# Optimization experiments

Measured on AMD Instinct MI355X. Metric: run time of the kernel, lower is better.

The kernel has to match this reference:

```python
import jax, jax.numpy as jnp
import numpy as np

N_NODES = 50000
N_EDGES = 1600000
N_GRAPHS = 512
HID = 32
NEG_SLOPE = 0.2  # PyG GATConv default leaky_relu slope
EPS = 1e-16      # PyG softmax denominator epsilon


def setup_inputs() -> dict:
    key = jax.random.key(0)
    ks = jax.random.split(key, 12)
    x = jax.random.normal(ks[0], (N_NODES, 12), jnp.float32)
    edge_index = jax.random.randint(ks[1], (2, N_EDGES), 0, N_NODES)
    edge_attr = jax.random.normal(ks[2], (N_EDGES, 3), jnp.float32)
    batch = jnp.sort(jax.random.randint(ks[3], (N_NODES,), 0, N_GRAPHS))
    g = lambda k, shp: jax.random.normal(k, shp, jnp.float32) * (1.0 / np.sqrt(shp[0]))
    return {
        "x": x, "edge_index": edge_index, "edge_attr": edge_attr, "batch": batch,
        "W": g(ks[4], (12, HID)),
        "att_src": g(ks[5], (HID,)), "att_dst": g(ks[6], (HID,)),
        "W_edge": g(ks[7], (3, HID)), "att_edge": g(ks[8], (HID,)),
        "bias": jnp.zeros((HID,), jnp.float32),
        "W_gate": g(ks[9], (HID, 1)), "b_gate": jnp.zeros((1,), jnp.float32),
        "W_out": g(ks[10], (HID, 1)), "b_out": jnp.zeros((1,), jnp.float32),
    }


def reference(x, edge_index, edge_attr, batch, W, att_src, att_dst, W_edge,
              att_edge, bias, W_gate, b_gate, W_out, b_out):
    N = x.shape[0]
    src, dst = edge_index[0], edge_index[1]

    # --- add self loops, edge_attr fill_value='mean' (mean of incoming edge attrs per node)
    deg = jax.ops.segment_sum(jnp.ones_like(edge_attr[:, 0]), dst, num_segments=N)
    loop_attr = jax.ops.segment_sum(edge_attr, dst, num_segments=N) / jnp.maximum(deg, 1.0)[:, None]
    loop = jnp.arange(N, dtype=src.dtype)
    src_f = jnp.concatenate([src, loop])
    dst_f = jnp.concatenate([dst, loop])
    ea = jnp.concatenate([edge_attr, loop_attr], axis=0)  # [E+N, 3]

    # --- GATConv (heads=1)
    h = x @ W                       # [N, HID]
    a_src = h @ att_src             # [N]
    a_dst = h @ att_dst             # [N]
    a_edge = (ea @ W_edge) @ att_edge  # [E+N]
    alpha = jax.nn.leaky_relu(a_src[src_f] + a_dst[dst_f] + a_edge, NEG_SLOPE)
    # segment softmax over destination neighborhoods
    m = jax.ops.segment_max(alpha, dst_f, num_segments=N)
    e = jnp.exp(alpha - m[dst_f])
    z = jax.ops.segment_sum(e, dst_f, num_segments=N)
    alpha = e / (z[dst_f] + EPS)
    out = jax.ops.segment_sum(h[src_f] * alpha[:, None], dst_f, num_segments=N) + bias

    out = jax.nn.relu(out)  # dropout is identity in eval mode

    # --- GlobalAttention pooling: gate = softmax(Linear(out), batch)
    gate = (out @ W_gate + b_gate)[:, 0]  # [N]
    gm = jax.ops.segment_max(gate, batch, num_segments=N_GRAPHS)
    ge = jnp.exp(gate - gm[batch])
    gz = jax.ops.segment_sum(ge, batch, num_segments=N_GRAPHS)
    gate = ge / (gz[batch] + EPS)
    pooled = jax.ops.segment_sum(out * gate[:, None], batch, num_segments=N_GRAPHS)  # [G, HID]

    return jax.nn.sigmoid(pooled @ W_out + b_out)  # [G, 1]
```

## Files before the change

kernel.cpp:

```cpp
#include <hip/hip_runtime.h>
#include <hip/hip_fp16.h>
#include <math.h>

#define N_NODES 50000
#define N_EDGES 1600000
#define N_GRAPHS 512
#define HID 32
#define NEG_SLOPE 0.2f
#define SM_EPS 1e-16f
#define PAD 80
#define NBIN 511
#define BIN_W 98
#define BIN_CAP 3800
#define EPT 10
#define PART_BLOCKS 313
#define MAXG 8

__global__ __launch_bounds__(512) void k_part_node(const int* __restrict__ ei,
                                                   const float* __restrict__ ea,
                                                   const float* __restrict__ W_edge,
                                                   const float* __restrict__ att_edge,
                                                   const float* __restrict__ x,
                                                   const float* __restrict__ W,
                                                   const float* __restrict__ att_src,
                                                   const float* __restrict__ att_dst,
                                                   uint2* __restrict__ part,
                                                   int* __restrict__ pcur,
                                                   __half2* __restrict__ h2,
                                                   float* __restrict__ a_src,
                                                   float* __restrict__ a_dst) {
    __shared__ float sv[3];
    __shared__ float sW[12 * 32], sas[32], sad[32];
    __shared__ int lcnt[NBIN], lcur[NBIN];
    int t = threadIdx.x;
    if (t < 3) {
        float v = 0.f;
        for (int j = 0; j < 32; ++j) v += W_edge[t * 32 + j] * att_edge[j];
        sv[t] = v;
    }
    for (int i = t; i < 12 * 32; i += 512) sW[i] = W[i];
    if (t < 32) { sas[t] = att_src[t]; sad[t] = att_dst[t]; }
    for (int i = t; i < NBIN; i += 512) lcnt[i] = 0;
    __syncthreads();

    uint2 r[EPT];
    int bin[EPT];
    int ebase = blockIdx.x * (512 * EPT) + t;
#pragma unroll
    for (int i = 0; i < EPT; ++i) {
        int e = ebase + i * 512;
        if (e < N_EDGES) {
            int s = ei[e];
            int d = ei[N_EDGES + e];
            float aev = ea[e * 3 + 0] * sv[0] + ea[e * 3 + 1] * sv[1] + ea[e * 3 + 2] * sv[2];
            r[i] = make_uint2((unsigned)d | ((unsigned)s << 16), __float_as_uint(aev));
            bin[i] = d / BIN_W;
            atomicAdd(&lcnt[bin[i]], 1);
        } else {
            bin[i] = -1;
        }
    }
    __syncthreads();
    for (int i = t; i < NBIN; i += 512) lcur[i] = atomicAdd(pcur + i, lcnt[i]);
    __syncthreads();
#pragma unroll
    for (int i = 0; i < EPT; ++i) {
        if (bin[i] >= 0) {
            int pos = atomicAdd(&lcur[bin[i]], 1);
            if (pos < BIN_CAP) part[(size_t)bin[i] * BIN_CAP + pos] = r[i];
        }
    }

    int n = blockIdx.x * 160 + t;
    if (t < 160 && n < N_NODES) {
        float xv[12];
#pragma unroll
        for (int j = 0; j < 12; ++j) xv[j] = x[n * 12 + j];
        float hv[32];
        float as = 0.f, ad = 0.f;
#pragma unroll
        for (int k = 0; k < 32; ++k) {
            float acc = 0.f;
#pragma unroll
            for (int j = 0; j < 12; ++j) acc += xv[j] * sW[j * 32 + k];
            hv[k] = acc;
            as += acc * sas[k];
            ad += acc * sad[k];
        }
        a_src[n] = as;
        a_dst[n] = ad;
        __half2 hp[16];
#pragma unroll
        for (int k = 0; k < 16; ++k) hp[k] = __floats2half2_rn(hv[2 * k], hv[2 * k + 1]);
        uint4* dst = (uint4*)(h2 + (size_t)n * 16);
        const uint4* srcp = (const uint4*)hp;
#pragma unroll
        for (int k = 0; k < 4; ++k) dst[k] = srcp[k];
    }
}

__global__ __launch_bounds__(1024) void k_asm_gather(const uint2* __restrict__ part,
                                                     const int* __restrict__ pcur,
                                                     const __half2* __restrict__ h2,
                                                     const float* __restrict__ a_src,
                                                     const float* __restrict__ a_dst,
                                                     const float* __restrict__ bias,
                                                     const float* __restrict__ W_gate,
                                                     const float* __restrict__ b_gate,
                                                     const int* __restrict__ batch,
                                                     float* __restrict__ Sg,
                                                     float* __restrict__ gzg) {
    int b = blockIdx.x;
    int lo = b * BIN_W;
    if (lo >= N_NODES) return;
    int hi = lo + BIN_W; if (hi > N_NODES) hi = N_NODES;
    int nrow = hi - lo;
    __shared__ int lcur[BIN_W];
    __shared__ unsigned lbuck[BIN_W * PAD];
    __shared__ float S_local[MAXG][32];
    __shared__ float gz_local[MAXG];
    __shared__ int sgf, sgl;
    int t = threadIdx.x;
    if (t < BIN_W) lcur[t] = 0;
    if (t < MAXG * 32) S_local[t >> 5][t & 31] = 0.f;
    if (t < MAXG) gz_local[t] = 0.f;
    if (t == 0) { sgf = batch[lo]; sgl = batch[hi - 1]; }
    __syncthreads();
    int gfirst = sgf;

    int cnt = pcur[b]; if (cnt > BIN_CAP) cnt = BIN_CAP;
    const uint2* p = part + (size_t)b * BIN_CAP;
    for (int i = t; i < cnt; i += 1024) {
        uint2 r = p[i];
        int li = (int)(r.x & 0xFFFF) - lo;
        unsigned s = r.x >> 16;
        unsigned short hb = __half_as_ushort(__float2half_rn(__uint_as_float(r.y)));
        int pos = atomicAdd(&lcur[li], 1);
        if (pos < PAD) lbuck[li * PAD + pos] = s | ((unsigned)hb << 16);
    }
    __syncthreads();

    int l = t & 63, wl = t >> 6;
    int es = l >> 2;
    int cg = l & 3;
    float bg0 = b_gate[0];

    for (int li = wl; li < nrow; li += 16) {
        int n = lo + li;
        int deg_full = lcur[li];
        int degc = deg_full < PAD ? deg_full : PAD;
        float adst_n = a_dst[n];
        const unsigned* row = lbuck + li * PAD;

        float c0 = 0.f, c1 = 0.f, c2 = 0.f, c3 = 0.f, c4 = 0.f, c5 = 0.f, c6 = 0.f, c7 = 0.f;
        float wsum = 0.f, aevsum = 0.f;
        int j = es;
        for (; j + 16 < degc; j += 32) {
            unsigned p0 = row[j], p1 = row[j + 16];
            int s0 = p0 & 0xFFFF, s1 = p1 & 0xFFFF;
            float aev0 = __half2float(__ushort_as_half((unsigned short)(p0 >> 16)));
            float aev1 = __half2float(__ushort_as_half((unsigned short)(p1 >> 16)));
            float as0 = a_src[s0], as1 = a_src[s1];
            const uint4 u0 = *(const uint4*)(h2 + (size_t)s0 * 16 + cg * 4);
            const uint4 u1 = *(const uint4*)(h2 + (size_t)s1 * 16 + cg * 4);
            float a0 = as0 + adst_n + aev0; a0 = a0 > 0.f ? a0 : NEG_SLOPE * a0;
            float a1 = as1 + adst_n + aev1; a1 = a1 > 0.f ? a1 : NEG_SLOPE * a1;
            float w0 = __expf(a0), w1 = __expf(a1);
            wsum += w0 + w1; aevsum += aev0 + aev1;
            float2 f;
            f = __half22float2(*(const __half2*)&u0.x); c0 += w0 * f.x; c1 += w0 * f.y;
            f = __half22float2(*(const __half2*)&u0.y); c2 += w0 * f.x; c3 += w0 * f.y;
            f = __half22float2(*(const __half2*)&u0.z); c4 += w0 * f.x; c5 += w0 * f.y;
            f = __half22float2(*(const __half2*)&u0.w); c6 += w0 * f.x; c7 += w0 * f.y;
            f = __half22float2(*(const __half2*)&u1.x); c0 += w1 * f.x; c1 += w1 * f.y;
            f = __half22float2(*(const __half2*)&u1.y); c2 += w1 * f.x; c3 += w1 * f.y;
            f = __half22float2(*(const __half2*)&u1.z); c4 += w1 * f.x; c5 += w1 * f.y;
            f = __half22float2(*(const __half2*)&u1.w); c6 += w1 * f.x; c7 += w1 * f.y;
        }
        if (j < degc) {
            unsigned p0 = row[j];
            int s0 = p0 & 0xFFFF;
            float aev0 = __half2float(__ushort_as_half((unsigned short)(p0 >> 16)));
            float a0 = a_src[s0] + adst_n + aev0; a0 = a0 > 0.f ? a0 : NEG_SLOPE * a0;
            float w0 = __expf(a0);
            const uint4 u0 = *(const uint4*)(h2 + (size_t)s0 * 16 + cg * 4);
            wsum += w0; aevsum += aev0;
            float2 f;
            f = __half22float2(*(const __half2*)&u0.x); c0 += w0 * f.x; c1 += w0 * f.y;
            f = __half22float2(*(const __half2*)&u0.y); c2 += w0 * f.x; c3 += w0 * f.y;
            f = __half22float2(*(const __half2*)&u0.z); c4 += w0 * f.x; c5 += w0 * f.y;
            f = __half22float2(*(const __half2*)&u0.w); c6 += w0 * f.x; c7 += w0 * f.y;
        }

#pragma unroll
        for (int m = 4; m <= 32; m <<= 1) {
            c0 += __shfl_xor(c0, m); c1 += __shfl_xor(c1, m);
            c2 += __shfl_xor(c2, m); c3 += __shfl_xor(c3, m);
            c4 += __shfl_xor(c4, m); c5 += __shfl_xor(c5, m);
            c6 += __shfl_xor(c6, m); c7 += __shfl_xor(c7, m);
            wsum += __shfl_xor(wsum, m); aevsum += __shfl_xor(aevsum, m);
        }

        float dgm = deg_full > 1 ? (float)deg_full : 1.f;
        float al = a_src[n] + adst_n + aevsum / dgm;
        al = al > 0.f ? al : NEG_SLOPE * al;
        float el = __expf(al);
        float zi = 1.f / (wsum + el + SM_EPS);

        if (es == 0) {
            const uint4 un = *(const uint4*)(h2 + (size_t)n * 16 + cg * 4);
            float hn[8];
            float2 f;
            f = __half22float2(*(const __half2*)&un.x); hn[0] = f.x; hn[1] = f.y;
            f = __half22float2(*(const __half2*)&un.y); hn[2] = f.x; hn[3] = f.y;
            f = __half22float2(*(const __half2*)&un.z); hn[4] = f.x; hn[5] = f.y;
            f = __half22float2(*(const __half2*)&un.w); hn[6] = f.x; hn[7] = f.y;
            const float4 bva = *(const float4*)(bias + cg * 8);
            const float4 bvb = *(const float4*)(bias + cg * 8 + 4);
            float v[8];
            v[0] = (c0 + el * hn[0]) * zi + bva.x;
            v[1] = (c1 + el * hn[1]) * zi + bva.y;
            v[2] = (c2 + el * hn[2]) * zi + bva.z;
            v[3] = (c3 + el * hn[3]) * zi + bva.w;
            v[4] = (c4 + el * hn[4]) * zi + bvb.x;
            v[5] = (c5 + el * hn[5]) * zi + bvb.y;
            v[6] = (c6 + el * hn[6]) * zi + bvb.z;
            v[7] = (c7 + el * hn[7]) * zi + bvb.w;
#pragma unroll
            for (int k = 0; k < 8; ++k) v[k] = v[k] > 0.f ? v[k] : 0.f;
            const float4 wga = *(const float4*)(W_gate + cg * 8);
            const float4 wgb = *(const float4*)(W_gate + cg * 8 + 4);
            float g = v[0] * wga.x + v[1] * wga.y + v[2] * wga.z + v[3] * wga.w
                    + v[4] * wgb.x + v[5] * wgb.y + v[6] * wgb.z + v[7] * wgb.w;
            g += __shfl_xor(g, 1);
            g += __shfl_xor(g, 2);
            float gen = __expf(g + bg0);
            int gi = batch[n] - gfirst; gi = gi < MAXG - 1 ? gi : MAXG - 1;
#pragma unroll
            for (int k = 0; k < 8; ++k) atomicAdd(&S_local[gi][cg * 8 + k], gen * v[k]);
            if (cg == 0) atomicAdd(&gz_local[gi], gen);
        }
    }
    __syncthreads();

    int ngr = sgl - gfirst + 1; if (ngr > MAXG) ngr = MAXG;
    for (int i = t; i < ngr * 33; i += 1024) {
        int q = i / 33, c = i % 33;
        if (c < 32) atomicAdd(&Sg[(size_t)(gfirst + q) * 32 + c], S_local[q][c]);
        else atomicAdd(&gzg[gfirst + q], gz_local[q]);
    }
}

__global__ __launch_bounds__(256) void k_out(const float* __restrict__ Sg,
                                             const float* __restrict__ gzg,
                                             const float* __restrict__ W_out,
                                             const float* __restrict__ b_out,
                                             float* __restrict__ out) {
    int g = blockIdx.x * blockDim.x + threadIdx.x;
    if (g >= N_GRAPHS) return;
    float zi = 1.f / (gzg[g] + SM_EPS);
    float acc = b_out[0];
#pragma unroll
    for (int k = 0; k < 32; ++k) acc += Sg[(size_t)g * 32 + k] * zi * W_out[k];
    out[g] = 1.f / (1.f + __expf(-acc));
}

extern "C" void kernel_launch(void* const* d_in, const int* in_sizes, int n_in,
                              void* d_out, int out_size, void* d_ws, size_t ws_size,
                              hipStream_t stream) {
    const float* x        = (const float*)d_in[0];
    const int*   ei       = (const int*)  d_in[1];
    const float* ea       = (const float*)d_in[2];
    const int*   batch    = (const int*)  d_in[3];
    const float* W        = (const float*)d_in[4];
    const float* att_src  = (const float*)d_in[5];
    const float* att_dst  = (const float*)d_in[6];
    const float* W_edge   = (const float*)d_in[7];
    const float* att_edge = (const float*)d_in[8];
    const float* bias     = (const float*)d_in[9];
    const float* W_gate   = (const float*)d_in[10];
    const float* b_gate   = (const float*)d_in[11];
    const float* W_out    = (const float*)d_in[12];
    const float* b_out    = (const float*)d_in[13];
    float* out = (float*)d_out;

    char* wsb = (char*)d_ws;
    uint2*    part_  = (uint2*)wsb;
    __half2*  h2     = (__half2*)(part_ + (size_t)NBIN * BIN_CAP);
    float*    a_src  = (float*)(h2 + (size_t)16 * N_NODES);
    float*    a_dst  = a_src + N_NODES;
    float*    Sg     = a_dst + N_NODES;
    float*    gzg    = Sg + (size_t)N_GRAPHS * 32;
    int*      pcur   = (int*)(gzg + N_GRAPHS);

    size_t zero_bytes = ((size_t)N_GRAPHS * 33 + NBIN) * sizeof(float);
    hipMemsetAsync(Sg, 0, zero_bytes, stream);

    k_part_node<<<PART_BLOCKS, 512, 0, stream>>>(ei, ea, W_edge, att_edge, x, W, att_src,
                                                 att_dst, part_, pcur, h2, a_src, a_dst);
    k_asm_gather<<<NBIN, 1024, 0, stream>>>(part_, pcur, h2, a_src, a_dst, bias,
                                            W_gate, b_gate, batch, Sg, gzg);
    k_out<<<(N_GRAPHS + 255) / 256, 256, 0, stream>>>(Sg, gzg, W_out, b_out, out);
}
```

Measured before the change: 167.7 us.

## Stage partitioned edges in shared memory via local scan before global scatter

Each block now records a per-edge rank within its bin, prefix-scans the bin counts, and writes its edges into a shared-memory buffer sorted by bin. It then copies them to the global partition array with consecutive threads writing consecutive slots of a bin. The aim is to replace scattered 8-byte global writes with more coalesced runs and to drop the second round of shared atomics. The cost is about 40KB of extra shared memory, which may lower occupancy, plus a log-step scan with many barriers.

```diff
diff --git a/kernel.cpp b/kernel.cpp
--- a/kernel.cpp
+++ b/kernel.cpp
@@ -13,6 +13,7 @@
 #define BIN_W 98
 #define BIN_CAP 3800
 #define EPT 10
+#define EPB 5120
 #define PART_BLOCKS 313
 #define MAXG 8
 
@@ -31,7 +32,9 @@
                                                    float* __restrict__ a_dst) {
     __shared__ float sv[3];
     __shared__ float sW[12 * 32], sas[32], sad[32];
-    __shared__ int lcnt[NBIN], lcur[NBIN];
+    __shared__ int lcnt[NBIN], lbase[NBIN], lcur[NBIN];
+    __shared__ int sscan[512];
+    __shared__ uint2 sbuf[EPB];
     int t = threadIdx.x;
     if (t < 3) {
         float v = 0.f;
@@ -40,12 +43,12 @@
     }
     for (int i = t; i < 12 * 32; i += 512) sW[i] = W[i];
     if (t < 32) { sas[t] = att_src[t]; sad[t] = att_dst[t]; }
-    for (int i = t; i < NBIN; i += 512) lcnt[i] = 0;
+    if (t < NBIN) lcnt[t] = 0;
     __syncthreads();
 
     uint2 r[EPT];
-    int bin[EPT];
-    int ebase = blockIdx.x * (512 * EPT) + t;
+    int bin[EPT], rank[EPT];
+    int ebase = blockIdx.x * EPB + t;
 #pragma unroll
     for (int i = 0; i < EPT; ++i) {
         int e = ebase + i * 512;
@@ -55,20 +58,39 @@
             float aev = ea[e * 3 + 0] * sv[0] + ea[e * 3 + 1] * sv[1] + ea[e * 3 + 2] * sv[2];
             r[i] = make_uint2((unsigned)d | ((unsigned)s << 16), __float_as_uint(aev));
             bin[i] = d / BIN_W;
-            atomicAdd(&lcnt[bin[i]], 1);
+            rank[i] = atomicAdd(&lcnt[bin[i]], 1);
         } else {
             bin[i] = -1;
         }
     }
     __syncthreads();
-    for (int i = t; i < NBIN; i += 512) lcur[i] = atomicAdd(pcur + i, lcnt[i]);
-    __syncthreads();
-#pragma unroll
-    for (int i = 0; i < EPT; ++i) {
-        if (bin[i] >= 0) {
-            int pos = atomicAdd(&lcur[bin[i]], 1);
-            if (pos < BIN_CAP) part[(size_t)bin[i] * BIN_CAP + pos] = r[i];
-        }
+
+    int v = (t < NBIN) ? lcnt[t] : 0;
+    sscan[t] = v;
+    __syncthreads();
+    for (int ofs = 1; ofs < 512; ofs <<= 1) {
+        int u = (t >= ofs) ? sscan[t - ofs] : 0;
+        __syncthreads();
+        sscan[t] += u;
+        __syncthreads();
+    }
+    if (t < NBIN) {
+        lbase[t] = sscan[t] - v;
+        lcur[t] = atomicAdd(pcur + t, v);
+    }
+    __syncthreads();
+
+#pragma unroll
+    for (int i = 0; i < EPT; ++i)
+        if (bin[i] >= 0) sbuf[lbase[bin[i]] + rank[i]] = r[i];
+    __syncthreads();
+
+    int total = sscan[511];
+    for (int i = t; i < total; i += 512) {
+        uint2 e = sbuf[i];
+        int bb = (int)(e.x & 0xFFFF) / BIN_W;
+        int pos = lcur[bb] + (i - lbase[bb]);
+        if (pos < BIN_CAP) part[(size_t)bb * BIN_CAP + pos] = e;
     }
 
     int n = blockIdx.x * 160 + t;
```

After: 162.6 us. 3.1% less time.
